# Performance work log

Hardware: AMD Instinct MI355X
Metric: run time of the kernel (lower is better)

Reference implementation:

```python
import jax, jax.numpy as jnp
import numpy as np

BETA = 0.1
EPS = 1e-8  # F.cosine_similarity default eps


def setup_inputs() -> dict:
    key = jax.random.key(0)
    k1, k2 = jax.random.split(key)
    B, S, D = 32, 512, 1024
    fix_outputs = jax.random.normal(k1, (B, S, D), dtype=jnp.float32)
    region_mask = jax.random.randint(k2, (B, D), 0, 2) > 0  # bool feature mask
    return {"fix_outputs": fix_outputs, "region_mask": region_mask}


def reference(fix_outputs, region_mask):
    # fix_outputs: [B, S, D], region_mask: [B, D] bool (masks feature dims)
    B, S, D = fix_outputs.shape
    m = region_mask[:, None, :].astype(fix_outputs.dtype)      # [B, 1, D]
    x = fix_outputs * m                                         # masked features
    # Gram matrix of masked dot products over all time pairs: [B, S, S]
    G = jnp.einsum('btd,bud->btu', x, x)
    # per-timestep masked norms come from the diagonal
    n = jnp.sqrt(jnp.maximum(jnp.diagonal(G, axis1=1, axis2=2), 0.0))  # [B, S]
    n = jnp.maximum(n, EPS)
    sim = G / (n[:, :, None] * n[:, None, :])                   # cosine sims
    # the triple loop covers every pair (t, t+num_moves), num_moves>=1 ->
    # strict upper triangle of the [S, S] pair matrix for every batch element
    triu = jnp.triu(jnp.ones((S, S), dtype=bool), k=1)
    total = jnp.sum(jnp.where(triu[None, :, :], sim, 0.0))
    count = B * S * (S - 1) // 2
    avg = total / count
    return -jnp.log(1.0 - 0.5 * (avg + 1.0)) * BETA
```

## Files before the change

### kernel.cpp

```cpp
#include <hip/hip_runtime.h>
#include <math.h>

#define B_ 32
#define S_ 512
#define D_ 1024
#define EPS_ 1e-8f
#define BETA_ 0.1
#define NCH 32
#define TCH (S_ / NCH)


__device__ __forceinline__ float mask_val(const void* mp, int lay, int idx) {
  if (lay == 1) return ((const unsigned char*)mp)[idx] ? 1.0f : 0.0f;
  if (lay == 2) return (((const float*)mp)[idx] != 0.0f) ? 1.0f : 0.0f;
  return ((const int*)mp)[idx] ? 1.0f : 0.0f;
}

__device__ __forceinline__ float wave_sum_f(float v) {
#pragma unroll
  for (int off = 32; off > 0; off >>= 1) v += __shfl_down(v, off);
  return v;
}
__device__ __forceinline__ double wave_sum_d(double v) {
#pragma unroll
  for (int off = 32; off > 0; off >>= 1) v += __shfl_down(v, off);
  return v;
}

__device__ __forceinline__ int detect_layout(const void* mask, int tid,
                                             int* sflags) {
  if (tid == 0) *sflags = 0;
  __syncthreads();
  unsigned int w = ((const unsigned int*)mask)[tid & 255];
  int f = 0;
  if (w == 0x3F800000u) f = 2;
  else if (w > 1u) f = 1;
  if (f && (tid < 256)) atomicOr(sflags, f);
  __syncthreads();
  const int fl = *sflags;
  return (fl & 1) ? 1 : ((fl & 2) ? 2 : 0);
}

__global__ __launch_bounds__(256) void fused_kernel(
    const float* __restrict__ fix, const void* __restrict__ mask,
    float* __restrict__ part, float* __restrict__ diagpart) {
  const int b = blockIdx.x / NCH;
  const int ch = blockIdx.x % NCH;
  const int tid = threadIdx.x;

  __shared__ int sflags;
  const int lay = detect_layout(mask, tid, &sflags);

  const int mb = b * D_ + tid * 4;
  float4 m4;
  m4.x = mask_val(mask, lay, mb + 0);
  m4.y = mask_val(mask, lay, mb + 1);
  m4.z = mask_val(mask, lay, mb + 2);
  m4.w = mask_val(mask, lay, mb + 3);

  const float4* base =
      (const float4*)(fix + ((size_t)b * S_ + (size_t)ch * TCH) * D_);

  __shared__ float red[4];
  float4 acc = make_float4(0.0f, 0.0f, 0.0f, 0.0f);
  float diag = 0.0f;

  float4 v = base[tid];
  for (int t = 0; t < TCH; ++t) {
    float4 vn = make_float4(0.0f, 0.0f, 0.0f, 0.0f);
    if (t + 1 < TCH) vn = base[(size_t)(t + 1) * (D_ / 4) + tid];

    float ssq = v.x * v.x * m4.x + v.y * v.y * m4.y +
                v.z * v.z * m4.z + v.w * v.w * m4.w;
    ssq = wave_sum_f(ssq);
    if ((tid & 63) == 0) red[tid >> 6] = ssq;
    __syncthreads();
    const float s = red[0] + red[1] + red[2] + red[3];
    const float inv = 1.0f / fmaxf(sqrtf(fmaxf(s, 0.0f)), EPS_);
    acc.x += v.x * inv; acc.y += v.y * inv;
    acc.z += v.z * inv; acc.w += v.w * inv;
    diag += s * inv * inv;
    v = vn;
    __syncthreads();
  }

  ((float4*)(part + (size_t)ch * (B_ * D_) + (size_t)b * D_))[tid] = acc;
  if (tid == 0) diagpart[blockIdx.x] = diag;
}

__global__ __launch_bounds__(256) void reduce_kernel(
    const float* __restrict__ part, const void* __restrict__ mask,
    const float* __restrict__ diagpart, double* __restrict__ blkout) {
  const int tid = threadIdx.x;
  const int gid = blockIdx.x * 256 + tid;

  __shared__ int sflags;
  const int lay = detect_layout(mask, tid, &sflags);

  float s = 0.0f;
#pragma unroll
  for (int c = 0; c < NCH; ++c) s += part[c * (B_ * D_) + gid];
  const float sm = s * mask_val(mask, lay, gid);
  double full = (double)sm * (double)sm;
  full = wave_sum_d(full);
  __shared__ double redf[4];
  if ((tid & 63) == 0) redf[tid >> 6] = full;
  __syncthreads();
  if (tid == 0) {
    double dg = 0.0;
#pragma unroll
    for (int k = 0; k < 8; ++k) dg += (double)diagpart[blockIdx.x * 8 + k];
    blkout[blockIdx.x * 2 + 0] = redf[0] + redf[1] + redf[2] + redf[3];
    blkout[blockIdx.x * 2 + 1] = dg;
  }
}

__global__ __launch_bounds__(128) void final_kernel(
    const double* __restrict__ blkout, float* __restrict__ out) {
  const int tid = threadIdx.x;
  double f = blkout[tid * 2 + 0];
  double g = blkout[tid * 2 + 1];
  f = wave_sum_d(f);
  g = wave_sum_d(g);
  __shared__ double rf[2], rg[2];
  if ((tid & 63) == 0) { rf[tid >> 6] = f; rg[tid >> 6] = g; }
  __syncthreads();
  if (tid == 0) {
    const double F = rf[0] + rf[1];
    const double G = rg[0] + rg[1];
    const double total = 0.5 * (F - G);
    const double count = (double)B_ * S_ * (S_ - 1) / 2.0;
    const double avg = total / count;
    const double val = -log(1.0 - 0.5 * (avg + 1.0)) * BETA_;
    out[0] = (float)val;
  }
}

extern "C" void kernel_launch(void* const* d_in, const int* in_sizes, int n_in,
                              void* d_out, int out_size, void* d_ws, size_t ws_size,
                              hipStream_t stream) {
  const float* fix = (const float*)d_in[0];
  const void* mask = d_in[1];
  char* ws = (char*)d_ws;

  float* part     = (float*)ws;
  float* diagpart = (float*)(ws + (size_t)NCH * B_ * D_ * 4);
  double* blkout  = (double*)(ws + (size_t)NCH * B_ * D_ * 4 + 8192);

  float* out = (float*)d_out;

  fused_kernel<<<B_ * NCH, 256, 0, stream>>>(fix, mask, part, diagpart);
  reduce_kernel<<<(B_ * D_) / 256, 256, 0, stream>>>(part, mask, diagpart, blkout);
  final_kernel<<<1, 128, 0, stream>>>(blkout, out);
}
```

Baseline: 22.93 us.

## Give each wave its own rows and fuse the final reduction via a last-block counter

The first kernel now assigns each wave to 4 whole rows, so the per-row norm is an xor-shuffle wave reduction with no block barriers inside the row loop. Partial sums from the four waves are combined through shared memory at the end. The separate final kernel is replaced by a last-block-done pattern: an atomic counter, reset by the first kernel, lets the final reduce block compute the output. This removes one launch and many syncthreads, at the cost of more registers per thread and reliance on threadfence and atomic ordering.

```diff
diff --git a/kernel.cpp b/kernel.cpp
--- a/kernel.cpp
+++ b/kernel.cpp
@@ -7,7 +7,8 @@
 #define EPS_ 1e-8f
 #define BETA_ 0.1
 #define NCH 32
-#define TCH (S_ / NCH)
+#define TCH 16
+#define RPW 4
 
 
 __device__ __forceinline__ float mask_val(const void* mp, int lay, int idx) {
@@ -16,14 +17,14 @@
   return ((const int*)mp)[idx] ? 1.0f : 0.0f;
 }
 
-__device__ __forceinline__ float wave_sum_f(float v) {
-#pragma unroll
-  for (int off = 32; off > 0; off >>= 1) v += __shfl_down(v, off);
+__device__ __forceinline__ float wave_allsum_f(float v) {
+#pragma unroll
+  for (int off = 32; off > 0; off >>= 1) v += __shfl_xor(v, off);
   return v;
 }
-__device__ __forceinline__ double wave_sum_d(double v) {
-#pragma unroll
-  for (int off = 32; off > 0; off >>= 1) v += __shfl_down(v, off);
+__device__ __forceinline__ double wave_allsum_d(double v) {
+#pragma unroll
+  for (int off = 32; off > 0; off >>= 1) v += __shfl_xor(v, off);
   return v;
 }
 
@@ -31,11 +32,11 @@
                                              int* sflags) {
   if (tid == 0) *sflags = 0;
   __syncthreads();
-  unsigned int w = ((const unsigned int*)mask)[tid & 255];
+  unsigned int wv = ((const unsigned int*)mask)[tid & 255];
   int f = 0;
-  if (w == 0x3F800000u) f = 2;
-  else if (w > 1u) f = 1;
-  if (f && (tid < 256)) atomicOr(sflags, f);
+  if (wv == 0x3F800000u) f = 2;
+  else if (wv > 1u) f = 1;
+  if (f) atomicOr(sflags, f);
   __syncthreads();
   const int fl = *sflags;
   return (fl & 1) ? 1 : ((fl & 2) ? 2 : 0);
@@ -43,56 +44,97 @@
 
 __global__ __launch_bounds__(256) void fused_kernel(
     const float* __restrict__ fix, const void* __restrict__ mask,
-    float* __restrict__ part, float* __restrict__ diagpart) {
-  const int b = blockIdx.x / NCH;
-  const int ch = blockIdx.x % NCH;
+    float* __restrict__ part, float* __restrict__ diagpart,
+    unsigned int* __restrict__ counter) {
+  const int blk = blockIdx.x;
+  const int b = blk >> 5;
+  const int ch = blk & 31;
   const int tid = threadIdx.x;
+  const int w = tid >> 6;
+  const int lane = tid & 63;
+
+  if (blk == 0 && tid == 0) *counter = 0u;
 
   __shared__ int sflags;
   const int lay = detect_layout(mask, tid, &sflags);
 
-  const int mb = b * D_ + tid * 4;
-  float4 m4;
-  m4.x = mask_val(mask, lay, mb + 0);
-  m4.y = mask_val(mask, lay, mb + 1);
-  m4.z = mask_val(mask, lay, mb + 2);
-  m4.w = mask_val(mask, lay, mb + 3);
-
-  const float4* base =
-      (const float4*)(fix + ((size_t)b * S_ + (size_t)ch * TCH) * D_);
-
-  __shared__ float red[4];
-  float4 acc = make_float4(0.0f, 0.0f, 0.0f, 0.0f);
+  float4 m4[4];
+  const int mrow = b * D_;
+#pragma unroll
+  for (int k = 0; k < 4; ++k) {
+    const int c0 = mrow + (lane + 64 * k) * 4;
+    m4[k].x = mask_val(mask, lay, c0 + 0);
+    m4[k].y = mask_val(mask, lay, c0 + 1);
+    m4[k].z = mask_val(mask, lay, c0 + 2);
+    m4[k].w = mask_val(mask, lay, c0 + 3);
+  }
+
+  const float4* rowbase = (const float4*)(
+      fix + ((size_t)b * S_ + (size_t)ch * TCH + (size_t)w * RPW) * D_);
+
+  float4 acc[4];
+#pragma unroll
+  for (int k = 0; k < 4; ++k) acc[k] = make_float4(0.f, 0.f, 0.f, 0.f);
   float diag = 0.0f;
 
-  float4 v = base[tid];
-  for (int t = 0; t < TCH; ++t) {
-    float4 vn = make_float4(0.0f, 0.0f, 0.0f, 0.0f);
-    if (t + 1 < TCH) vn = base[(size_t)(t + 1) * (D_ / 4) + tid];
-
-    float ssq = v.x * v.x * m4.x + v.y * v.y * m4.y +
-                v.z * v.z * m4.z + v.w * v.w * m4.w;
-    ssq = wave_sum_f(ssq);
-    if ((tid & 63) == 0) red[tid >> 6] = ssq;
-    __syncthreads();
-    const float s = red[0] + red[1] + red[2] + red[3];
-    const float inv = 1.0f / fmaxf(sqrtf(fmaxf(s, 0.0f)), EPS_);
-    acc.x += v.x * inv; acc.y += v.y * inv;
-    acc.z += v.z * inv; acc.w += v.w * inv;
-    diag += s * inv * inv;
-    v = vn;
-    __syncthreads();
-  }
-
-  ((float4*)(part + (size_t)ch * (B_ * D_) + (size_t)b * D_))[tid] = acc;
-  if (tid == 0) diagpart[blockIdx.x] = diag;
-}
-
-__global__ __launch_bounds__(256) void reduce_kernel(
+  float4 v[4];
+#pragma unroll
+  for (int k = 0; k < 4; ++k) v[k] = rowbase[lane + 64 * k];
+
+  for (int i = 0; i < RPW; ++i) {
+    float4 vn[4];
+    if (i + 1 < RPW) {
+#pragma unroll
+      for (int k = 0; k < 4; ++k)
+        vn[k] = rowbase[(size_t)(i + 1) * (D_ / 4) + lane + 64 * k];
+    } else {
+#pragma unroll
+      for (int k = 0; k < 4; ++k) vn[k] = v[k];
+    }
+    float ssq = 0.f;
+#pragma unroll
+    for (int k = 0; k < 4; ++k)
+      ssq += v[k].x * v[k].x * m4[k].x + v[k].y * v[k].y * m4[k].y +
+             v[k].z * v[k].z * m4[k].z + v[k].w * v[k].w * m4[k].w;
+    ssq = wave_allsum_f(ssq);
+    const float inv = 1.0f / fmaxf(sqrtf(fmaxf(ssq, 0.0f)), EPS_);
+#pragma unroll
+    for (int k = 0; k < 4; ++k) {
+      acc[k].x += v[k].x * inv; acc[k].y += v[k].y * inv;
+      acc[k].z += v[k].z * inv; acc[k].w += v[k].w * inv;
+    }
+    diag += ssq * inv * inv;
+#pragma unroll
+    for (int k = 0; k < 4; ++k) v[k] = vn[k];
+  }
+
+  __shared__ float comb[4][D_];
+  __shared__ float sdiag[4];
+#pragma unroll
+  for (int k = 0; k < 4; ++k) ((float4*)comb[w])[lane + 64 * k] = acc[k];
+  if (lane == 0) sdiag[w] = diag;
+  __syncthreads();
+
+  const float4 s0 = ((const float4*)comb[0])[tid];
+  const float4 s1 = ((const float4*)comb[1])[tid];
+  const float4 s2 = ((const float4*)comb[2])[tid];
+  const float4 s3 = ((const float4*)comb[3])[tid];
+  float4 r;
+  r.x = (s0.x + s1.x) + (s2.x + s3.x);
+  r.y = (s0.y + s1.y) + (s2.y + s3.y);
+  r.z = (s0.z + s1.z) + (s2.z + s3.z);
+  r.w = (s0.w + s1.w) + (s2.w + s3.w);
+  ((float4*)(part + (size_t)ch * (B_ * D_) + (size_t)b * D_))[tid] = r;
+  if (tid == 0) diagpart[blk] = (sdiag[0] + sdiag[1]) + (sdiag[2] + sdiag[3]);
+}
+
+__global__ __launch_bounds__(256) void reduce_final_kernel(
     const float* __restrict__ part, const void* __restrict__ mask,
-    const float* __restrict__ diagpart, double* __restrict__ blkout) {
+    const float* __restrict__ diagpart, double* __restrict__ blkout,
+    unsigned int* __restrict__ counter, float* __restrict__ out) {
   const int tid = threadIdx.x;
-  const int gid = blockIdx.x * 256 + tid;
+  const int bid = blockIdx.x;
+  const int gid = bid * 256 + tid;
 
   __shared__ int sflags;
   const int lay = detect_layout(mask, tid, &sflags);
@@ -102,28 +144,37 @@
   for (int c = 0; c < NCH; ++c) s += part[c * (B_ * D_) + gid];
   const float sm = s * mask_val(mask, lay, gid);
   double full = (double)sm * (double)sm;
-  full = wave_sum_d(full);
+  full = wave_allsum_d(full);
   __shared__ double redf[4];
   if ((tid & 63) == 0) redf[tid >> 6] = full;
   __syncthreads();
+
+  __shared__ bool is_last;
   if (tid == 0) {
     double dg = 0.0;
 #pragma unroll
-    for (int k = 0; k < 8; ++k) dg += (double)diagpart[blockIdx.x * 8 + k];
-    blkout[blockIdx.x * 2 + 0] = redf[0] + redf[1] + redf[2] + redf[3];
-    blkout[blockIdx.x * 2 + 1] = dg;
-  }
-}
-
-__global__ __launch_bounds__(128) void final_kernel(
-    const double* __restrict__ blkout, float* __restrict__ out) {
-  const int tid = threadIdx.x;
-  double f = blkout[tid * 2 + 0];
-  double g = blkout[tid * 2 + 1];
-  f = wave_sum_d(f);
-  g = wave_sum_d(g);
+    for (int k = 0; k < 8; ++k) dg += (double)diagpart[bid * 8 + k];
+    blkout[bid * 2 + 0] = (redf[0] + redf[1]) + (redf[2] + redf[3]);
+    blkout[bid * 2 + 1] = dg;
+    __threadfence();
+    const unsigned int prev = atomicAdd(counter, 1u);
+    is_last = (prev == 127u);
+  }
+  __syncthreads();
+  if (!is_last) return;
+
+  __threadfence();
+  double f = 0.0, g = 0.0;
+  if (tid < 128) {
+    volatile double* vb = blkout;
+    f = vb[tid * 2 + 0];
+    g = vb[tid * 2 + 1];
+  }
+  f = wave_allsum_d(f);
+  g = wave_allsum_d(g);
   __shared__ double rf[2], rg[2];
-  if ((tid & 63) == 0) { rf[tid >> 6] = f; rg[tid >> 6] = g; }
+  if (tid == 0)  { rf[0] = f; rg[0] = g; }
+  if (tid == 64) { rf[1] = f; rg[1] = g; }
   __syncthreads();
   if (tid == 0) {
     const double F = rf[0] + rf[1];
@@ -131,8 +182,7 @@
     const double total = 0.5 * (F - G);
     const double count = (double)B_ * S_ * (S_ - 1) / 2.0;
     const double avg = total / count;
-    const double val = -log(1.0 - 0.5 * (avg + 1.0)) * BETA_;
-    out[0] = (float)val;
+    out[0] = (float)(-log(1.0 - 0.5 * (avg + 1.0)) * BETA_);
   }
 }
 
@@ -143,13 +193,15 @@
   const void* mask = d_in[1];
   char* ws = (char*)d_ws;
 
-  float* part     = (float*)ws;
-  float* diagpart = (float*)(ws + (size_t)NCH * B_ * D_ * 4);
-  double* blkout  = (double*)(ws + (size_t)NCH * B_ * D_ * 4 + 8192);
+  const size_t part_bytes = (size_t)NCH * B_ * D_ * sizeof(float);
+  float* part       = (float*)ws;
+  float* diagpart   = (float*)(ws + part_bytes);
+  double* blkout    = (double*)(ws + part_bytes + 8192);
+  unsigned int* cnt = (unsigned int*)(ws + part_bytes + 8192 + 4096);
 
   float* out = (float*)d_out;
 
-  fused_kernel<<<B_ * NCH, 256, 0, stream>>>(fix, mask, part, diagpart);
-  reduce_kernel<<<(B_ * D_) / 256, 256, 0, stream>>>(part, mask, diagpart, blkout);
-  final_kernel<<<1, 128, 0, stream>>>(blkout, out);
-}
+  fused_kernel<<<B_ * NCH, 256, 0, stream>>>(fix, mask, part, diagpart, cnt);
+  reduce_final_kernel<<<(B_ * D_) / 256, 256, 0, stream>>>(
+      part, mask, diagpart, blkout, cnt, out);
+}
```

Result: slower. 30.92 us (+34.8%).
